# Optimization experiments

Hardware: AMD Instinct MI355X
Metric: run time of the kernel (lower is better)

## Reference

```python
import jax, jax.numpy as jnp
import numpy as np

B, T, D, H = 4, 1024, 1024, 16
HD = D // H  # 64
EPS = 1e-5


def _layernorm(x, g, b):
    mu = jnp.mean(x, axis=-1, keepdims=True)
    var = jnp.mean(jnp.square(x - mu), axis=-1, keepdims=True)
    return (x - mu) * jax.lax.rsqrt(var + EPS) * g + b


def _apply_rope(x, cos, sin):
    # x: (B, H, T, HD); cos/sin: (T, HD//2)
    d = x.shape[-1] // 2
    x1, x2 = x[..., :d], x[..., d:]
    cos = cos[None, None]
    sin = sin[None, None]
    return jnp.concatenate([x1 * cos - x2 * sin, x1 * sin + x2 * cos], axis=-1)


def setup_inputs() -> dict:
    key = jax.random.key(0)
    ks = jax.random.split(key, 8)
    s = 0.02
    x = jax.random.normal(ks[0], (B, T, D), jnp.float32)
    # RoPE tables
    pos = jnp.arange(T, dtype=jnp.float32)
    inv_freq = 1.0 / (10000.0 ** (jnp.arange(HD // 2, dtype=jnp.float32) / (HD // 2)))
    ang = pos[:, None] * inv_freq[None, :]  # (T, HD//2)
    rope_cos, rope_sin = jnp.cos(ang), jnp.sin(ang)
    # causal mask: True = masked out (module does ~attn_mask before SDPA)
    attn_mask = jnp.triu(jnp.ones((T, T), dtype=bool), k=1)
    params = dict(
        ln1_g=jnp.ones((D,), jnp.float32), ln1_b=jnp.zeros((D,), jnp.float32),
        w_qkv=jax.random.normal(ks[1], (D, 3 * D), jnp.float32) * s,
        b_qkv=jnp.zeros((3 * D,), jnp.float32),
        w_out=jax.random.normal(ks[2], (D, D), jnp.float32) * s,
        b_out=jnp.zeros((D,), jnp.float32),
        ln2_g=jnp.ones((D,), jnp.float32), ln2_b=jnp.zeros((D,), jnp.float32),
        w1=jax.random.normal(ks[3], (D, 4 * D), jnp.float32) * s,
        b1=jnp.zeros((4 * D,), jnp.float32),
        w2=jax.random.normal(ks[4], (4 * D, D), jnp.float32) * s,
        b2=jnp.zeros((D,), jnp.float32),
    )
    return dict(x=x, attn_mask=attn_mask, rope_cos=rope_cos, rope_sin=rope_sin, **params)


def reference(x, attn_mask, rope_cos, rope_sin, ln1_g, ln1_b, w_qkv, b_qkv,
              w_out, b_out, ln2_g, ln2_b, w1, b1, w2, b2):
    b, t, d = x.shape
    h = _layernorm(x, ln1_g, ln1_b)
    qkv = (h @ w_qkv + b_qkv).reshape(b, t, 3, H, HD)
    q, k, v = jnp.transpose(qkv, (2, 0, 3, 1, 4))  # each (B, H, T, HD)
    q = _apply_rope(q, rope_cos, rope_sin)
    k = _apply_rope(k, rope_cos, rope_sin)
    scale = 1.0 / jnp.sqrt(jnp.asarray(HD, x.dtype))
    scores = jnp.einsum('bhqd,bhkd->bhqk', q, k) * scale
    allowed = ~attn_mask  # True = attend
    neg = jnp.finfo(scores.dtype).min
    scores = jnp.where(allowed[None, None], scores, neg)
    probs = jax.nn.softmax(scores, axis=-1)
    attn = jnp.einsum('bhqk,bhkd->bhqd', probs, v)
    attn = jnp.transpose(attn, (0, 2, 1, 3)).reshape(b, t, d)
    x = x + (attn @ w_out + b_out)
    h2 = _layernorm(x, ln2_g, ln2_b)
    mlp = jax.nn.gelu(h2 @ w1 + b1, approximate=False) @ w2 + b2
    return x + mlp
```

## Files before the change

### kernel.cpp

```cpp
#include <hip/hip_runtime.h>
#include <hip/hip_bf16.h>
#include <cstdint>


typedef __bf16 bf16x8_t __attribute__((ext_vector_type(8)));
typedef float  f32x4_t  __attribute__((ext_vector_type(4)));

#define MFMA16(a, b, c) __builtin_amdgcn_mfma_f32_16x16x32_bf16((a), (b), (c), 0, 0, 0)

static constexpr int Bb = 4, T = 1024, D = 1024, NH = 16, HD = 64;
static constexpr int ROWS = Bb * T;
static constexpr int QKVN = 3 * D;

__device__ __forceinline__ float bf2f(__hip_bfloat16 v) { return __bfloat162float(v); }
__device__ __forceinline__ ushort f2bfbits(float v) {
    __hip_bfloat16 h = __float2bfloat16(v);
    return *reinterpret_cast<ushort*>(&h);
}
__device__ __forceinline__ float loadf(const void* p, size_t i, int isb16) {
    return isb16 ? bf2f(((const __hip_bfloat16*)p)[i]) : ((const float*)p)[i];
}
__device__ __forceinline__ int dtype16(const void* gref) {
    return (((const unsigned*)gref)[0] & 0xFFFFu) != 0u;
}
__device__ __forceinline__ void gld_lds16(const __hip_bfloat16* g, __hip_bfloat16* l) {
    __builtin_amdgcn_global_load_lds(
        (const __attribute__((address_space(1))) void*)g,
        (__attribute__((address_space(3))) void*)l, 16, 0, 0);
}

__device__ __forceinline__ void trans_tile(const void* B, __hip_bfloat16* BT,
                                           int K, int N, int k0, int n0, int isb16) {
    __shared__ ushort t[64][65];
#pragma unroll
    for (int it = 0; it < 16; ++it) {
        int idx = threadIdx.x + it * 256;
        int r = idx >> 6, c = idx & 63;
        t[c][r] = f2bfbits(loadf(B, (size_t)(k0 + r) * N + n0 + c, isb16));
    }
    __syncthreads();
#pragma unroll
    for (int it = 0; it < 16; ++it) {
        int idx = threadIdx.x + it * 256;
        int r = idx >> 6, c = idx & 63;
        reinterpret_cast<ushort*>(BT)[(size_t)(n0 + r) * K + k0 + c] = t[r][c];
    }
}

__global__ __launch_bounds__(256) void transpose_k(const void* __restrict__ B,
                                                   __hip_bfloat16* __restrict__ BT,
                                                   const void* __restrict__ gref,
                                                   int K, int N) {
    trans_tile(B, BT, K, N, blockIdx.y * 64, blockIdx.x * 64, dtype16(gref));
}

__global__ __launch_bounds__(256) void megatrans_k(const void* w_qkv, const void* w_out,
                                                   const void* w1, const void* w2,
                                                   __hip_bfloat16* wqkvT, __hip_bfloat16* woutT,
                                                   __hip_bfloat16* w1T, __hip_bfloat16* w2T,
                                                   const void* __restrict__ gref) {
    const int isb16 = dtype16(gref);
    int bid = blockIdx.x;
    const void* src; __hip_bfloat16* dst; int K, N, l;
    if (bid < 768)       { src = w_qkv; dst = wqkvT; K = 1024; N = 3072; l = bid; }
    else if (bid < 1024) { src = w_out; dst = woutT; K = 1024; N = 1024; l = bid - 768; }
    else if (bid < 2048) { src = w1;    dst = w1T;   K = 1024; N = 4096; l = bid - 1024; }
    else                 { src = w2;    dst = w2T;   K = 4096; N = 1024; l = bid - 2048; }
    const int nb = N / 64;
    trans_tile(src, dst, K, N, (l / nb) * 64, (l % nb) * 64, isb16);
}

__global__ __launch_bounds__(256) void ln_k(const void* __restrict__ x,
                                            const void* __restrict__ g,
                                            const void* __restrict__ bt,
                                            __hip_bfloat16* __restrict__ out,
                                            const void* __restrict__ gref) {
    const int isb16 = dtype16(gref);
    const int row = blockIdx.x, tid = threadIdx.x;
    const int lane = tid & 63, w = tid >> 6;

    float v[4];
    if (isb16) {
        ushort4 raw = reinterpret_cast<const ushort4*>((const __hip_bfloat16*)x + (size_t)row * D)[tid];
        v[0] = __uint_as_float(((unsigned)raw.x) << 16);
        v[1] = __uint_as_float(((unsigned)raw.y) << 16);
        v[2] = __uint_as_float(((unsigned)raw.z) << 16);
        v[3] = __uint_as_float(((unsigned)raw.w) << 16);
    } else {
        float4 f = reinterpret_cast<const float4*>((const float*)x + (size_t)row * D)[tid];
        v[0] = f.x; v[1] = f.y; v[2] = f.z; v[3] = f.w;
    }

    float s1 = v[0] + v[1] + v[2] + v[3];
    float s2 = v[0] * v[0] + v[1] * v[1] + v[2] * v[2] + v[3] * v[3];
#pragma unroll
    for (int off = 32; off >= 1; off >>= 1) {
        s1 += __shfl_xor(s1, off, 64);
        s2 += __shfl_xor(s2, off, 64);
    }
    __shared__ float r1[4], r2[4];
    if (lane == 0) { r1[w] = s1; r2[w] = s2; }
    __syncthreads();
    float t1 = r1[0] + r1[1] + r1[2] + r1[3];
    float t2 = r2[0] + r2[1] + r2[2] + r2[3];
    float mu  = t1 * (1.0f / D);
    float var = t2 * (1.0f / D) - mu * mu;
    float rstd = rsqrtf(var + 1e-5f);

    const int c = tid * 4;
#pragma unroll
    for (int j = 0; j < 4; j++) {
        float gv = loadf(g, c + j, isb16), bv = loadf(bt, c + j, isb16);
        out[(size_t)row * D + c + j] = __float2bfloat16((v[j] - mu) * rstd * gv + bv);
    }
}

template <int MODE, bool SPLIT>
__global__ __launch_bounds__(512, 2) void gemm256_k(const __hip_bfloat16* __restrict__ A,
                                                    const __hip_bfloat16* __restrict__ BT,
                                                    const void* __restrict__ bias,
                                                    void* __restrict__ C,
                                                    const void* __restrict__ gref,
                                                    int M, int N, int Kstride, int klen) {
    extern __shared__ __hip_bfloat16 LDSb[];

    const int tid  = threadIdx.x;
    const int lane = tid & 63, w = tid >> 6;
    const int quad = lane >> 4, l15 = lane & 15;
    const int n0 = blockIdx.x * 256, m0 = blockIdx.y * 256;
    const int wmL = (w >> 2) * 128;
    const int wnL = (w & 3) * 64;
    const int kbase = SPLIT ? blockIdx.z * klen : 0;
    const int NT = klen >> 5;

    const int L0 = w * 1024 + lane * 16;
    const int L1 = L0 + 8192;
    const int r0 = L0 >> 6,  k0e = ((L0 & 63) ^ (((L0 >> 9) & 1) << 5)) >> 1;
    const int r1 = L1 >> 6,  k1e = ((L1 & 63) ^ (((L1 >> 9) & 1) << 5)) >> 1;
    const __hip_bfloat16* AgS0 = A  + (size_t)(m0 + r0) * Kstride + kbase + k0e;
    const __hip_bfloat16* AgS1 = A  + (size_t)(m0 + r1) * Kstride + kbase + k1e;
    const __hip_bfloat16* BgS0 = BT + (size_t)(n0 + r0) * Kstride + kbase + k0e;
    const __hip_bfloat16* BgS1 = BT + (size_t)(n0 + r1) * Kstride + kbase + k1e;
    const int ldst0 = w * 512, ldst1 = w * 512 + 4096;

    const int kofs = (quad * 8) ^ ((l15 & 8) << 1);

    f32x4_t acc[8][4] = {};

#pragma unroll
    for (int t = 0; t < 3; ++t) {
        __hip_bfloat16* sA = LDSb + t * 8192;
        __hip_bfloat16* sB = LDSb + 32768 + t * 8192;
        const int ko = t * 32;
        gld_lds16(AgS0 + ko, sA + ldst0);
        gld_lds16(AgS1 + ko, sA + ldst1);
        gld_lds16(BgS0 + ko, sB + ldst0);
        gld_lds16(BgS1 + ko, sB + ldst1);
    }
    asm volatile("s_waitcnt vmcnt(8)" ::: "memory");
    __builtin_amdgcn_s_barrier();
    __builtin_amdgcn_sched_barrier(0);

    for (int t = 0; t < NT; ++t) {
        if (t) {
            if (t + 2 < NT)      { asm volatile("s_waitcnt vmcnt(8)" ::: "memory"); }
            else if (t + 1 < NT) { asm volatile("s_waitcnt vmcnt(4)" ::: "memory"); }
            else                 { asm volatile("s_waitcnt vmcnt(0)" ::: "memory"); }
            __builtin_amdgcn_s_barrier();
            __builtin_amdgcn_sched_barrier(0);
        }

        const __hip_bfloat16* sA = LDSb + (t & 3) * 8192;
        const __hip_bfloat16* sB = LDSb + 32768 + (t & 3) * 8192;
        const bool pf = (t + 3 < NT);
        const int sl = (t + 3) & 3;
        __hip_bfloat16* nA = LDSb + sl * 8192;
        __hip_bfloat16* nB = LDSb + 32768 + sl * 8192;
        const int ko = (t + 3) * 32;

        bf16x8_t a[4], b[4];
#pragma unroll
        for (int mf = 0; mf < 4; ++mf)
            a[mf] = *reinterpret_cast<const bf16x8_t*>(&sA[(wmL + mf * 16 + l15) * 32 + kofs]);
#pragma unroll
        for (int nf = 0; nf < 4; ++nf)
            b[nf] = *reinterpret_cast<const bf16x8_t*>(&sB[(wnL + nf * 16 + l15) * 32 + kofs]);
        if (pf) {
            gld_lds16(AgS0 + ko, nA + ldst0);
            gld_lds16(AgS1 + ko, nA + ldst1);
        }
        __builtin_amdgcn_sched_barrier(0);
        __builtin_amdgcn_s_barrier();
        asm volatile("s_waitcnt lgkmcnt(0)" ::: "memory");
        __builtin_amdgcn_sched_barrier(0);
        __builtin_amdgcn_s_setprio(1);
#pragma unroll
        for (int mf = 0; mf < 4; ++mf)
#pragma unroll
            for (int nf = 0; nf < 4; ++nf)
                acc[mf][nf] = MFMA16(a[mf], b[nf], acc[mf][nf]);
        __builtin_amdgcn_s_setprio(0);
        __builtin_amdgcn_sched_barrier(0);
        __builtin_amdgcn_s_barrier();

        bf16x8_t a2[4];
#pragma unroll
        for (int mf = 0; mf < 4; ++mf)
            a2[mf] = *reinterpret_cast<const bf16x8_t*>(&sA[(wmL + 64 + mf * 16 + l15) * 32 + kofs]);
        if (pf) {
            gld_lds16(BgS0 + ko, nB + ldst0);
            gld_lds16(BgS1 + ko, nB + ldst1);
        }
        __builtin_amdgcn_sched_barrier(0);
        asm volatile("s_waitcnt lgkmcnt(0)" ::: "memory");
        __builtin_amdgcn_sched_barrier(0);
        __builtin_amdgcn_s_setprio(1);
#pragma unroll
        for (int mf = 0; mf < 4; ++mf)
#pragma unroll
            for (int nf = 0; nf < 4; ++nf)
                acc[4 + mf][nf] = MFMA16(a2[mf], b[nf], acc[4 + mf][nf]);
        __builtin_amdgcn_s_setprio(0);
        __builtin_amdgcn_sched_barrier(0);
    }

    __syncthreads();

    __hip_bfloat16* Cb;
    if constexpr (SPLIT) {
        const int z = blockIdx.z;
        if (z == 0)      Cb = (__hip_bfloat16*)C;
        else if (z == 1) Cb = (__hip_bfloat16*)C + (size_t)M * N;
        else if (z == 2) Cb = (__hip_bfloat16*)const_cast<void*>(bias);
        else             Cb = (__hip_bfloat16*)const_cast<void*>(gref);
    } else {
        Cb = (__hip_bfloat16*)C;
    }
    const int isb16 = (MODE == 3) ? 0 : dtype16(gref);
    __hip_bfloat16* E = LDSb;
#pragma unroll
    for (int nf = 0; nf < 4; ++nf) {
        const int cc = wnL + nf * 16 + l15;
        const float bsv = (MODE == 3) ? 0.0f : loadf(bias, n0 + cc, isb16);
#pragma unroll
        for (int mf = 0; mf < 8; ++mf) {
            const int rbase = wmL + mf * 16 + quad * 4;
#pragma unroll
            for (int r = 0; r < 4; ++r) {
                const int rr = rbase + r;
                float v = acc[mf][nf][r] + bsv;
                if constexpr (MODE == 2)
                    v = 0.5f * v * (1.0f + erff(v * 0.70710678118654752f));
                E[rr * 256 + ((cc + (((rr >> 2) & 15) << 4)) & 255)] = __float2bfloat16(v);
            }
        }
    }
    __syncthreads();
#pragma unroll
    for (int it = 0; it < 16; ++it) {
        const int r = it * 16 + (tid >> 5), c = (tid & 31) * 8;
        const int cs = (c + (((r >> 2) & 15) << 4)) & 255;
        uint4 d = *reinterpret_cast<const uint4*>(&E[r * 256 + cs]);
        *reinterpret_cast<uint4*>(&Cb[(size_t)(m0 + r) * N + n0 + c]) = d;
    }
}

template <int MODE, bool SPLIT>
__global__ __launch_bounds__(256) void gemm_k(const __hip_bfloat16* __restrict__ A,
                                              const __hip_bfloat16* __restrict__ BT,
                                              const void* __restrict__ bias,
                                              void* __restrict__ C,
                                              const void* __restrict__ gref,
                                              int M, int N, int Kstride, int klen) {
    __shared__ __hip_bfloat16 LB[16384];

    const int tid  = threadIdx.x;
    const int lane = tid & 63, w = tid >> 6;
    const int quad = lane >> 4, l15 = lane & 15;
    const int n0 = blockIdx.x * 128, m0 = blockIdx.y * 128;
    const int wm = (w >> 1) * 64, wn = (w & 1) * 64;
    const int kbase = SPLIT ? blockIdx.z * klen : 0;

    const int srow = lane >> 2, skk = (lane & 3) * 8;
    const __hip_bfloat16* Ag = A  + (size_t)(m0 + w * 16 + srow) * Kstride + kbase + skk;
    const __hip_bfloat16* Bg = BT + (size_t)(n0 + w * 16 + srow) * Kstride + kbase + skk;
    const int lwb = (w * 16) * 32;

    f32x4_t acc[4][4] = {};

    gld_lds16(Ag,                LB + lwb);
    gld_lds16(Ag + 64 * Kstride, LB + lwb + 64 * 32);
    gld_lds16(Bg,                LB + 8192 + lwb);
    gld_lds16(Bg + 64 * Kstride, LB + 8192 + lwb + 64 * 32);
    __syncthreads();

    int p = 0;
    for (int k0 = 0; k0 < klen; k0 += 32) {
        if (k0 + 32 < klen) {
            __hip_bfloat16* An = LB + (p ^ 1) * 4096;
            __hip_bfloat16* Bn = LB + 8192 + (p ^ 1) * 4096;
            gld_lds16(Ag + k0 + 32,                An + lwb);
            gld_lds16(Ag + k0 + 32 + 64 * Kstride, An + lwb + 64 * 32);
            gld_lds16(Bg + k0 + 32,                Bn + lwb);
            gld_lds16(Bg + k0 + 32 + 64 * Kstride, Bn + lwb + 64 * 32);
        }

        const __hip_bfloat16* Ac = LB + p * 4096;
        const __hip_bfloat16* Bc = LB + 8192 + p * 4096;
        bf16x8_t af[4], bfr[4];
#pragma unroll
        for (int t = 0; t < 4; t++) {
            af[t]  = *reinterpret_cast<const bf16x8_t*>(&Ac[(wm + t * 16 + l15) * 32 + quad * 8]);
            bfr[t] = *reinterpret_cast<const bf16x8_t*>(&Bc[(wn + t * 16 + l15) * 32 + quad * 8]);
        }
#pragma unroll
        for (int i = 0; i < 4; i++)
#pragma unroll
            for (int j = 0; j < 4; j++)
                acc[i][j] = MFMA16(af[i], bfr[j], acc[i][j]);

        __syncthreads();
        p ^= 1;
    }

    __hip_bfloat16* Cb;
    if constexpr (SPLIT) {
        const int z = blockIdx.z;
        if (z == 0)      Cb = (__hip_bfloat16*)C;
        else if (z == 1) Cb = (__hip_bfloat16*)C + (size_t)M * N;
        else if (z == 2) Cb = (__hip_bfloat16*)const_cast<void*>(bias);
        else             Cb = (__hip_bfloat16*)const_cast<void*>(gref);
    } else {
        Cb = (__hip_bfloat16*)C;
    }
    const int isb16 = (MODE == 3) ? 0 : dtype16(gref);
    __hip_bfloat16* E = LB;
#pragma unroll
    for (int j = 0; j < 4; j++) {
        const int cc = wn + j * 16 + l15;
        const float bsv = (MODE == 3) ? 0.0f : loadf(bias, n0 + cc, isb16);
#pragma unroll
        for (int i = 0; i < 4; i++) {
            const int rbase = wm + i * 16 + quad * 4;
#pragma unroll
            for (int r = 0; r < 4; r++) {
                const int rr = rbase + r;
                float v = acc[i][j][r] + bsv;
                if constexpr (MODE == 2)
                    v = 0.5f * v * (1.0f + erff(v * 0.70710678118654752f));
                E[rr * 128 + ((cc + (((rr >> 2) & 7) << 4)) & 127)] = __float2bfloat16(v);
            }
        }
    }
    __syncthreads();
#pragma unroll
    for (int it = 0; it < 8; it++) {
        const int r = it * 16 + (tid >> 4), c = (tid & 15) * 8;
        const int cs = (c + (((r >> 2) & 7) << 4)) & 127;
        uint4 d = *reinterpret_cast<const uint4*>(&E[r * 128 + cs]);
        *reinterpret_cast<uint4*>(&Cb[(size_t)(m0 + r) * N + n0 + c]) = d;
    }
}

__global__ __launch_bounds__(256) void reduce4_k(const __hip_bfloat16* __restrict__ p0,
                                                 const __hip_bfloat16* __restrict__ p1,
                                                 const __hip_bfloat16* __restrict__ p2,
                                                 const __hip_bfloat16* __restrict__ p3,
                                                 const void* __restrict__ bias,
                                                 const void* __restrict__ res,
                                                 void* __restrict__ out,
                                                 const void* __restrict__ gref) {
    const int isb16 = dtype16(gref);
    const size_t i = ((size_t)blockIdx.x * 256 + threadIdx.x) * 4;
    ushort4 a = *reinterpret_cast<const ushort4*>(p0 + i);
    ushort4 b = *reinterpret_cast<const ushort4*>(p1 + i);
    ushort4 c = *reinterpret_cast<const ushort4*>(p2 + i);
    ushort4 d = *reinterpret_cast<const ushort4*>(p3 + i);
    const int col = (int)(i & (D - 1));
    float v[4];
    v[0] = __uint_as_float((unsigned)a.x << 16) + __uint_as_float((unsigned)b.x << 16)
         + __uint_as_float((unsigned)c.x << 16) + __uint_as_float((unsigned)d.x << 16);
    v[1] = __uint_as_float((unsigned)a.y << 16) + __uint_as_float((unsigned)b.y << 16)
         + __uint_as_float((unsigned)c.y << 16) + __uint_as_float((unsigned)d.y << 16);
    v[2] = __uint_as_float((unsigned)a.z << 16) + __uint_as_float((unsigned)b.z << 16)
         + __uint_as_float((unsigned)c.z << 16) + __uint_as_float((unsigned)d.z << 16);
    v[3] = __uint_as_float((unsigned)a.w << 16) + __uint_as_float((unsigned)b.w << 16)
         + __uint_as_float((unsigned)c.w << 16) + __uint_as_float((unsigned)d.w << 16);
#pragma unroll
    for (int j = 0; j < 4; j++)
        v[j] += loadf(bias, col + j, isb16) + loadf(res, i + j, isb16);
    if (isb16) {
        ushort4 o;
        o.x = f2bfbits(v[0]); o.y = f2bfbits(v[1]); o.z = f2bfbits(v[2]); o.w = f2bfbits(v[3]);
        *reinterpret_cast<ushort4*>((__hip_bfloat16*)out + i) = o;
    } else {
        float4 o = {v[0], v[1], v[2], v[3]};
        *reinterpret_cast<float4*>((float*)out + i) = o;
    }
}

__global__ __launch_bounds__(256) void gemm64_k(const __hip_bfloat16* __restrict__ A,
                                                const __hip_bfloat16* __restrict__ BT,
                                                const void* __restrict__ bias,
                                                const void* __restrict__ res,
                                                void* __restrict__ C,
                                                const void* __restrict__ gref,
                                                int M, int N, int K, int crow0) {
    __shared__ __hip_bfloat16 LB64[12288];

    const int tid  = threadIdx.x;
    const int lane = tid & 63, w = tid >> 6;
    const int quad = lane >> 4, l15 = lane & 15;
    const int n0 = blockIdx.x * 64, m0 = blockIdx.y * 128;
    const int wm = (w >> 1) * 64, wn = (w & 1) * 32;

    const int srow = lane >> 2, skk = (lane & 3) * 8;
    const __hip_bfloat16* Ag = A  + (size_t)(m0 + w * 16 + srow) * K + skk;
    const __hip_bfloat16* Bg = BT + (size_t)(n0 + w * 16 + srow) * K + skk;
    const int lwb = (w * 16) * 32;

    f32x4_t acc[4][2] = {};

    gld_lds16(Ag,          LB64 + lwb);
    gld_lds16(Ag + 64 * K, LB64 + lwb + 64 * 32);
    gld_lds16(Bg,          LB64 + 8192 + lwb);
    __syncthreads();

    int p = 0;
    for (int k0 = 0; k0 < K; k0 += 32) {
        if (k0 + 32 < K) {
            __hip_bfloat16* An = LB64 + (p ^ 1) * 4096;
            __hip_bfloat16* Bn = LB64 + 8192 + (p ^ 1) * 2048;
            gld_lds16(Ag + k0 + 32,          An + lwb);
            gld_lds16(Ag + k0 + 32 + 64 * K, An + lwb + 64 * 32);
            gld_lds16(Bg + k0 + 32,          Bn + lwb);
        }

        const __hip_bfloat16* Ac = LB64 + p * 4096;
        const __hip_bfloat16* Bc = LB64 + 8192 + p * 2048;
        bf16x8_t af[4], bfr[2];
#pragma unroll
        for (int t = 0; t < 4; t++)
            af[t]  = *reinterpret_cast<const bf16x8_t*>(&Ac[(wm + t * 16 + l15) * 32 + quad * 8]);
#pragma unroll
        for (int t = 0; t < 2; t++)
            bfr[t] = *reinterpret_cast<const bf16x8_t*>(&Bc[(wn + t * 16 + l15) * 32 + quad * 8]);
#pragma unroll
        for (int i = 0; i < 4; i++)
#pragma unroll
            for (int j = 0; j < 2; j++)
                acc[i][j] = MFMA16(af[i], bfr[j], acc[i][j]);

        __syncthreads();
        p ^= 1;
    }

    const int isb16 = dtype16(gref);
#pragma unroll
    for (int j = 0; j < 2; j++) {
        const int col = n0 + wn + j * 16 + l15;
        const float bsv = loadf(bias, col, isb16);
#pragma unroll
        for (int i = 0; i < 4; i++) {
            const int rbase = m0 + wm + i * 16 + quad * 4;
#pragma unroll
            for (int r = 0; r < 4; r++) {
                const size_t gr = (size_t)(crow0 + rbase + r);
                float v = acc[i][j][r] + bsv + loadf(res, gr * N + col, isb16);
                if (isb16) ((__hip_bfloat16*)C)[gr * N + col] = __float2bfloat16(v);
                else       ((float*)C)[gr * N + col] = v;
            }
        }
    }
}

__global__ __launch_bounds__(256) void ropevt_k(__hip_bfloat16* __restrict__ qkv,
                                                const void* __restrict__ rc,
                                                const void* __restrict__ rs,
                                                __hip_bfloat16* __restrict__ vT,
                                                const void* __restrict__ gref) {
    const int bid = blockIdx.x;
    if (bid < 8192) {
        const int isb16 = dtype16(gref);
        const int id = bid * 256 + threadIdx.x;
        const int d  = id & 31;
        const int h  = (id >> 5) & 15;
        const int t  = (id >> 9) & 1023;
        const int b  = id >> 19;
        const float c = loadf(rc, t * 32 + d, isb16);
        const float s = loadf(rs, t * 32 + d, isb16);
        __hip_bfloat16* base = qkv + ((size_t)(b * T + t)) * QKVN + h * HD + d;
        float x1 = bf2f(base[0]), x2 = bf2f(base[32]);
        base[0]  = __float2bfloat16((x1 * c - x2 * s) * 0.125f);
        base[32] = __float2bfloat16((x1 * s + x2 * c) * 0.125f);
        float y1 = bf2f(base[D]), y2 = bf2f(base[D + 32]);
        base[D]      = __float2bfloat16(y1 * c - y2 * s);
        base[D + 32] = __float2bfloat16(y1 * s + y2 * c);
    } else {
        __shared__ ushort t[64][65];
        const int l = bid - 8192;
        const int t0 = (l & 15) * 64, bh = l >> 4;
        const int b = bh >> 4, h = bh & 15;
        const __hip_bfloat16* src = qkv + ((size_t)b * T) * QKVN + 2 * D + h * HD;
#pragma unroll
        for (int it = 0; it < 16; ++it) {
            int idx = threadIdx.x + it * 256;
            int r = idx >> 6, d = idx & 63;
            t[d][r] = *reinterpret_cast<const ushort*>(src + (size_t)(t0 + r) * QKVN + d);
        }
        __syncthreads();
#pragma unroll
        for (int it = 0; it < 16; ++it) {
            int idx = threadIdx.x + it * 256;
            int r = idx >> 6, c = idx & 63;
            reinterpret_cast<ushort*>(vT)[((size_t)bh * 64 + r) * T + t0 + c] = t[r][c];
        }
    }
}

__global__ __launch_bounds__(256) void flash_k(const __hip_bfloat16* __restrict__ qkv,
                                               const __hip_bfloat16* __restrict__ vT,
                                               __hip_bfloat16* __restrict__ out) {
    __shared__ __hip_bfloat16 Qs[2][64 * 32];
    __shared__ __hip_bfloat16 Ks[2][2][64 * 32];
    __shared__ __hip_bfloat16 Vs[2][2][64 * 32];
    __shared__ __hip_bfloat16 Ps[4][2][16 * 32];

    const int tid = threadIdx.x;
    const int bid = blockIdx.x;
    const int qt = 15 - (bid >> 6);
    const int bh = bid & 63;
    const int b = bh >> 4, h = bh & 15;
    const int q0 = qt * 64;
    const int lane = tid & 63, w = tid >> 6, quad = lane >> 4, l15 = lane & 15;
    const int srow = lane >> 2, skk = (lane & 3) * 8;

    const __hip_bfloat16* qg = qkv + ((size_t)(b * T) + q0 + w * 16 + srow) * QKVN + h * HD + skk;
    const __hip_bfloat16* kg = qkv + ((size_t)(b * T) + w * 16 + srow) * QKVN + D + h * HD + skk;
    const __hip_bfloat16* vg = vT + ((size_t)bh * 64 + w * 16 + srow) * T + skk;

    gld_lds16(qg,      &Qs[0][(w * 16) * 32]);
    gld_lds16(qg + 32, &Qs[1][(w * 16) * 32]);
    gld_lds16(kg,      &Ks[0][0][(w * 16) * 32]);
    gld_lds16(kg + 32, &Ks[0][1][(w * 16) * 32]);
    gld_lds16(vg,      &Vs[0][0][(w * 16) * 32]);
    gld_lds16(vg + 32, &Vs[0][1][(w * 16) * 32]);
    __syncthreads();

    const bf16x8_t aq0 = *reinterpret_cast<const bf16x8_t*>(&Qs[0][(w * 16 + l15) * 32 + quad * 8]);
    const bf16x8_t aq1 = *reinterpret_cast<const bf16x8_t*>(&Qs[1][(w * 16 + l15) * 32 + quad * 8]);

    float m_run[4], l_run[4];
    f32x4_t o[4] = {};
#pragma unroll
    for (int i = 0; i < 4; i++) { m_run[i] = -1e30f; l_run[i] = 0.0f; }

    int p = 0;
    for (int kt = 0; kt <= qt; kt++) {
        if (kt < qt) {
            const size_t ko = (size_t)(kt + 1) * 64;
            gld_lds16(kg + ko * QKVN,      &Ks[p ^ 1][0][(w * 16) * 32]);
            gld_lds16(kg + ko * QKVN + 32, &Ks[p ^ 1][1][(w * 16) * 32]);
            gld_lds16(vg + ko,             &Vs[p ^ 1][0][(w * 16) * 32]);
            gld_lds16(vg + ko + 32,        &Vs[p ^ 1][1][(w * 16) * 32]);
        }

        f32x4_t s[4];
#pragma unroll
        for (int c = 0; c < 4; c++) {
            f32x4_t z = {};
            bf16x8_t k0f = *reinterpret_cast<const bf16x8_t*>(&Ks[p][0][(c * 16 + l15) * 32 + quad * 8]);
            bf16x8_t k1f = *reinterpret_cast<const bf16x8_t*>(&Ks[p][1][(c * 16 + l15) * 32 + quad * 8]);
            z = MFMA16(aq0, k0f, z);
            z = MFMA16(aq1, k1f, z);
            s[c] = z;
        }

        if (kt == qt) {
#pragma unroll
            for (int c = 0; c < 4; c++)
#pragma unroll
                for (int i = 0; i < 4; i++) {
                    int rr = w * 16 + quad * 4 + i;
                    int cc = c * 16 + l15;
                    if (cc > rr) s[c][i] = -1e30f;
                }
        }

        float mnew[4], alpha[4];
#pragma unroll
        for (int i = 0; i < 4; i++) {
            float mx = fmaxf(fmaxf(s[0][i], s[1][i]), fmaxf(s[2][i], s[3][i]));
#pragma unroll
            for (int off = 1; off < 16; off <<= 1) mx = fmaxf(mx, __shfl_xor(mx, off, 64));
            mnew[i] = fmaxf(m_run[i], mx);
            alpha[i] = __expf(m_run[i] - mnew[i]);
            m_run[i] = mnew[i];
        }
#pragma unroll
        for (int c = 0; c < 4; c++)
#pragma unroll
            for (int i = 0; i < 4; i++) s[c][i] = __expf(s[c][i] - mnew[i]);
#pragma unroll
        for (int i = 0; i < 4; i++) {
            float sm = s[0][i] + s[1][i] + s[2][i] + s[3][i];
#pragma unroll
            for (int off = 1; off < 16; off <<= 1) sm += __shfl_xor(sm, off, 64);
            l_run[i] = l_run[i] * alpha[i] + sm;
#pragma unroll
            for (int od = 0; od < 4; od++) o[od][i] *= alpha[i];
        }

#pragma unroll
        for (int c = 0; c < 4; c++)
#pragma unroll
            for (int i = 0; i < 4; i++)
                Ps[w][c >> 1][(quad * 4 + i) * 32 + (c & 1) * 16 + l15] =
                    __float2bfloat16(s[c][i]);

        bf16x8_t ap0 = *reinterpret_cast<const bf16x8_t*>(&Ps[w][0][l15 * 32 + quad * 8]);
        bf16x8_t ap1 = *reinterpret_cast<const bf16x8_t*>(&Ps[w][1][l15 * 32 + quad * 8]);
#pragma unroll
        for (int od = 0; od < 4; od++) {
            bf16x8_t v0f = *reinterpret_cast<const bf16x8_t*>(&Vs[p][0][(od * 16 + l15) * 32 + quad * 8]);
            bf16x8_t v1f = *reinterpret_cast<const bf16x8_t*>(&Vs[p][1][(od * 16 + l15) * 32 + quad * 8]);
            o[od] = MFMA16(ap0, v0f, o[od]);
            o[od] = MFMA16(ap1, v1f, o[od]);
        }

        __syncthreads();
        p ^= 1;
    }

#pragma unroll
    for (int od = 0; od < 4; od++)
#pragma unroll
        for (int i = 0; i < 4; i++) {
            int row = q0 + w * 16 + quad * 4 + i;
            int col = h * HD + od * 16 + l15;
            float v = o[od][i] / l_run[i];
            out[((size_t)b * T + row) * D + col] = __float2bfloat16(v);
        }
}

extern "C" void kernel_launch(void* const* d_in, const int* in_sizes, int n_in,
                              void* d_out, int out_size, void* d_ws, size_t ws_size,
                              hipStream_t stream) {
    const int o = (in_sizes[1] == T * (HD / 2)) ? 1 : 2;
    const void* x     = d_in[0];
    const void* rc    = d_in[o + 0];
    const void* rs    = d_in[o + 1];
    const void* ln1g  = d_in[o + 2];
    const void* ln1b  = d_in[o + 3];
    const void* w_qkv = d_in[o + 4];
    const void* b_qkv = d_in[o + 5];
    const void* w_out = d_in[o + 6];
    const void* b_out = d_in[o + 7];
    const void* ln2g  = d_in[o + 8];
    const void* ln2b  = d_in[o + 9];
    const void* w1    = d_in[o + 10];
    const void* b1    = d_in[o + 11];
    const void* w2    = d_in[o + 12];
    const void* b2    = d_in[o + 13];

    char* ws = (char*)d_ws;
    const size_t MB = 1024 * 1024;

    static bool attr_done = false;
    if (!attr_done) {
        hipFuncSetAttribute(reinterpret_cast<const void*>(&gemm256_k<0, false>),
                            hipFuncAttributeMaxDynamicSharedMemorySize, 131072);
        hipFuncSetAttribute(reinterpret_cast<const void*>(&gemm256_k<2, false>),
                            hipFuncAttributeMaxDynamicSharedMemorySize, 131072);
        hipFuncSetAttribute(reinterpret_cast<const void*>(&gemm256_k<3, true>),
                            hipFuncAttributeMaxDynamicSharedMemorySize, 131072);
        attr_done = true;
    }

    if (ws_size >= 72 * MB + 256) {
        __hip_bfloat16* bufA  = (__hip_bfloat16*)(ws + 256);
        __hip_bfloat16* qkvb  = (__hip_bfloat16*)(ws + 8 * MB + 256);
        __hip_bfloat16* vTb   = (__hip_bfloat16*)(ws + 32 * MB + 256);
        __hip_bfloat16* mid   = qkvb;
        __hip_bfloat16* wqkvT = (__hip_bfloat16*)(ws + 40 * MB + 256);
        __hip_bfloat16* woutT = (__hip_bfloat16*)(ws + 46 * MB + 256);
        __hip_bfloat16* w1T   = (__hip_bfloat16*)(ws + 48 * MB + 256);
        __hip_bfloat16* w2T   = (__hip_bfloat16*)(ws + 56 * MB + 256);
        __hip_bfloat16* part0 = (__hip_bfloat16*)(ws + 40 * MB + 256);
        __hip_bfloat16* part2 = (__hip_bfloat16*)(ws + 64 * MB + 256);
        __hip_bfloat16* part1 = (__hip_bfloat16*)(ws + 48 * MB + 256);
        __hip_bfloat16* part3 = bufA;

        megatrans_k<<<3072, 256, 0, stream>>>(w_qkv, w_out, w1, w2,
                                              wqkvT, woutT, w1T, w2T, ln1g);
        ln_k<<<ROWS, 256, 0, stream>>>(x, ln1g, ln1b, bufA, ln1g);
        gemm256_k<0, false><<<dim3(QKVN / 256, ROWS / 256), 512, 131072, stream>>>(
            bufA, wqkvT, b_qkv, qkvb, ln1g, ROWS, QKVN, D, D);
        ropevt_k<<<8192 + 1024, 256, 0, stream>>>(qkvb, rc, rs, vTb, ln1g);
        flash_k<<<16 * Bb * NH, 256, 0, stream>>>(qkvb, vTb, bufA);
        gemm64_k<<<dim3(D / 64, ROWS / 128), 256, 0, stream>>>(bufA, woutT, b_out, x,
                                                               d_out, ln1g, ROWS, D, D, 0);
        ln_k<<<ROWS, 256, 0, stream>>>(d_out, ln2g, ln2b, bufA, ln1g);
        gemm256_k<2, false><<<dim3(4 * D / 256, ROWS / 256), 512, 131072, stream>>>(
            bufA, w1T, b1, mid, ln1g, ROWS, 4 * D, D, D);
        gemm256_k<3, true><<<dim3(D / 256, ROWS / 256, 4), 512, 131072, stream>>>(
            mid, w2T, part2, part0, part3, ROWS, D, 4 * D, D);
        reduce4_k<<<(ROWS * D) / (256 * 4), 256, 0, stream>>>(part0, part1, part2, part3,
                                                              b2, d_out, d_out, ln1g);
    } else {
        __hip_bfloat16* bufA  = (__hip_bfloat16*)(ws + 256);
        __hip_bfloat16* qkvb  = (__hip_bfloat16*)(ws + 8 * MB + 256);
        __hip_bfloat16* wqkvT = (__hip_bfloat16*)(ws + 32 * MB + 256);
        __hip_bfloat16* vTb   = (__hip_bfloat16*)(ws + 32 * MB + 256);
        __hip_bfloat16* woutT = (__hip_bfloat16*)(ws + 8 * MB + 256);
        __hip_bfloat16* w1T   = (__hip_bfloat16*)(ws + 8 * MB + 256);
        __hip_bfloat16* w2T   = (__hip_bfloat16*)(ws + 16 * MB + 256);
        __hip_bfloat16* mid   = (__hip_bfloat16*)(ws + 24 * MB + 256);

        transpose_k<<<dim3(QKVN / 64, D / 64), 256, 0, stream>>>(w_qkv, wqkvT, ln1g, D, QKVN);
        ln_k<<<ROWS, 256, 0, stream>>>(x, ln1g, ln1b, bufA, ln1g);
        gemm_k<0, false><<<dim3(QKVN / 128, ROWS / 128), 256, 0, stream>>>(
            bufA, wqkvT, b_qkv, qkvb, ln1g, ROWS, QKVN, D, D);
        ropevt_k<<<8192 + 1024, 256, 0, stream>>>(qkvb, rc, rs, vTb, ln1g);
        flash_k<<<16 * Bb * NH, 256, 0, stream>>>(qkvb, vTb, bufA);
        transpose_k<<<dim3(D / 64, D / 64), 256, 0, stream>>>(w_out, woutT, ln1g, D, D);
        gemm64_k<<<dim3(D / 64, ROWS / 128), 256, 0, stream>>>(bufA, woutT, b_out, x,
                                                               d_out, ln1g, ROWS, D, D, 0);
        ln_k<<<ROWS, 256, 0, stream>>>(d_out, ln2g, ln2b, bufA, ln1g);
        transpose_k<<<dim3(4 * D / 64, D / 64), 256, 0, stream>>>(w1, w1T, ln1g, D, 4 * D);
        transpose_k<<<dim3(D / 64, 4 * D / 64), 256, 0, stream>>>(w2, w2T, ln1g, 4 * D, D);
        for (int c = 0; c < 2; c++) {
            const int ro = c * 2048;
            gemm_k<2, false><<<dim3(4 * D / 128, 2048 / 128), 256, 0, stream>>>(
                bufA + (size_t)ro * D, w1T, b1, mid, ln1g, 2048, 4 * D, D, D);
            gemm64_k<<<dim3(D / 64, 2048 / 128), 256, 0, stream>>>(mid, w2T, b2, d_out,
                                                                   d_out, ln1g, 2048, D, 4 * D, ro);
        }
    }
}
```

Baseline: 374.5 us.

## Restructure GEMM main loop to K=64 double-buffered four-phase pipeline with XCD-aware tile remap

```diff
diff --git a/kernel.cpp b/kernel.cpp
--- a/kernel.cpp
+++ b/kernel.cpp
@@ -127,68 +127,71 @@
     const int tid  = threadIdx.x;
     const int lane = tid & 63, w = tid >> 6;
     const int quad = lane >> 4, l15 = lane & 15;
-    const int n0 = blockIdx.x * 256, m0 = blockIdx.y * 256;
+
+    const int gx = gridDim.x;
+    const int nwg = gx * gridDim.y;
+    const int id = (int)blockIdx.y * gx + (int)blockIdx.x;
+    const int cpx = nwg >> 3;
+    const int sid = (id & 7) * cpx + (id >> 3);
+    const int n0 = (sid % gx) * 256, m0 = (sid / gx) * 256;
+
     const int wmL = (w >> 2) * 128;
     const int wnL = (w & 3) * 64;
     const int kbase = SPLIT ? blockIdx.z * klen : 0;
-    const int NT = klen >> 5;
-
-    const int L0 = w * 1024 + lane * 16;
-    const int L1 = L0 + 8192;
-    const int r0 = L0 >> 6,  k0e = ((L0 & 63) ^ (((L0 >> 9) & 1) << 5)) >> 1;
-    const int r1 = L1 >> 6,  k1e = ((L1 & 63) ^ (((L1 >> 9) & 1) << 5)) >> 1;
-    const __hip_bfloat16* AgS0 = A  + (size_t)(m0 + r0) * Kstride + kbase + k0e;
-    const __hip_bfloat16* AgS1 = A  + (size_t)(m0 + r1) * Kstride + kbase + k1e;
-    const __hip_bfloat16* BgS0 = BT + (size_t)(n0 + r0) * Kstride + kbase + k0e;
-    const __hip_bfloat16* BgS1 = BT + (size_t)(n0 + r1) * Kstride + kbase + k1e;
-    const int ldst0 = w * 512, ldst1 = w * 512 + 4096;
-
-    const int kofs = (quad * 8) ^ ((l15 & 8) << 1);
+    const int NT = klen >> 6;
+
+    const int gcol = 8 * ((lane & 7) ^ ((lane >> 3) & 7));
+    const __hip_bfloat16* AgS = A  + (size_t)(m0 + w * 8 + (lane >> 3)) * Kstride + kbase + gcol;
+    const __hip_bfloat16* BgS = BT + (size_t)(n0 + w * 8 + (lane >> 3)) * Kstride + kbase + gcol;
+    const int ldst = w * 512;
+
+    auto stgA = [&](int tt, int hi) {
+        __hip_bfloat16* d = LDSb + (tt & 1) * 16384 + hi * 8192 + ldst;
+        const __hip_bfloat16* g = AgS + (size_t)(hi * 128) * Kstride + (size_t)tt * 64;
+        gld_lds16(g,                          d);
+        gld_lds16(g + (size_t)64 * Kstride,   d + 4096);
+    };
+    auto stgB = [&](int tt, int hi) {
+        __hip_bfloat16* d = LDSb + 32768 + (tt & 1) * 16384 + hi * 8192 + ldst;
+        const __hip_bfloat16* g = BgS + (size_t)(hi * 128) * Kstride + (size_t)tt * 64;
+        gld_lds16(g,                          d);
+        gld_lds16(g + (size_t)64 * Kstride,   d + 4096);
+    };
+
+    const int cSw = (quad * 8) ^ ((l15 & 7) << 3);
+    auto rdA = [&](int as_, int row, int kk) -> bf16x8_t {
+        return *reinterpret_cast<const bf16x8_t*>(&LDSb[as_ + row * 64 + (cSw ^ (kk << 5))]);
+    };
+    auto rdB = [&](int bs_, int row, int kk) -> bf16x8_t {
+        return *reinterpret_cast<const bf16x8_t*>(&LDSb[bs_ + row * 64 + (cSw ^ (kk << 5))]);
+    };
 
     f32x4_t acc[8][4] = {};
 
-#pragma unroll
-    for (int t = 0; t < 3; ++t) {
-        __hip_bfloat16* sA = LDSb + t * 8192;
-        __hip_bfloat16* sB = LDSb + 32768 + t * 8192;
-        const int ko = t * 32;
-        gld_lds16(AgS0 + ko, sA + ldst0);
-        gld_lds16(AgS1 + ko, sA + ldst1);
-        gld_lds16(BgS0 + ko, sB + ldst0);
-        gld_lds16(BgS1 + ko, sB + ldst1);
-    }
-    asm volatile("s_waitcnt vmcnt(8)" ::: "memory");
+    stgA(0, 0); stgA(0, 1); stgB(0, 0); stgB(0, 1);
+    if (NT > 1) { stgB(1, 0); stgB(1, 1); }
+    if (NT > 1) { asm volatile("s_waitcnt vmcnt(4)" ::: "memory"); }
+    else        { asm volatile("s_waitcnt vmcnt(0)" ::: "memory"); }
     __builtin_amdgcn_s_barrier();
     __builtin_amdgcn_sched_barrier(0);
 
     for (int t = 0; t < NT; ++t) {
-        if (t) {
-            if (t + 2 < NT)      { asm volatile("s_waitcnt vmcnt(8)" ::: "memory"); }
-            else if (t + 1 < NT) { asm volatile("s_waitcnt vmcnt(4)" ::: "memory"); }
-            else                 { asm volatile("s_waitcnt vmcnt(0)" ::: "memory"); }
-            __builtin_amdgcn_s_barrier();
-            __builtin_amdgcn_sched_barrier(0);
-        }
-
-        const __hip_bfloat16* sA = LDSb + (t & 3) * 8192;
-        const __hip_bfloat16* sB = LDSb + 32768 + (t & 3) * 8192;
-        const bool pf = (t + 3 < NT);
-        const int sl = (t + 3) & 3;
-        __hip_bfloat16* nA = LDSb + sl * 8192;
-        __hip_bfloat16* nB = LDSb + 32768 + sl * 8192;
-        const int ko = (t + 3) * 32;
-
-        bf16x8_t a[4], b[4];
+        const int as = (t & 1) * 16384;
+        const int bs = 32768 + (t & 1) * 16384;
+        bf16x8_t aF[8], bF[8];
+
 #pragma unroll
         for (int mf = 0; mf < 4; ++mf)
-            a[mf] = *reinterpret_cast<const bf16x8_t*>(&sA[(wmL + mf * 16 + l15) * 32 + kofs]);
-#pragma unroll
-        for (int nf = 0; nf < 4; ++nf)
-            b[nf] = *reinterpret_cast<const bf16x8_t*>(&sB[(wnL + nf * 16 + l15) * 32 + kofs]);
-        if (pf) {
-            gld_lds16(AgS0 + ko, nA + ldst0);
-            gld_lds16(AgS1 + ko, nA + ldst1);
-        }
+#pragma unroll
+            for (int kk = 0; kk < 2; ++kk)
+                aF[mf * 2 + kk] = rdA(as, wmL + mf * 16 + l15, kk);
+#pragma unroll
+        for (int nf = 0; nf < 2; ++nf)
+#pragma unroll
+            for (int kk = 0; kk < 2; ++kk)
+                bF[nf * 2 + kk] = rdB(bs, wnL + nf * 16 + l15, kk);
+        if (t + 1 < NT) stgA(t + 1, 0);
+        asm volatile("s_waitcnt lgkmcnt(8)" ::: "memory");
         __builtin_amdgcn_sched_barrier(0);
         __builtin_amdgcn_s_barrier();
         asm volatile("s_waitcnt lgkmcnt(0)" ::: "memory");
@@ -197,31 +200,74 @@
 #pragma unroll
         for (int mf = 0; mf < 4; ++mf)
 #pragma unroll
-            for (int nf = 0; nf < 4; ++nf)
-                acc[mf][nf] = MFMA16(a[mf], b[nf], acc[mf][nf]);
+            for (int nf = 0; nf < 2; ++nf)
+#pragma unroll
+                for (int kk = 0; kk < 2; ++kk)
+                    acc[mf][nf] = MFMA16(aF[mf * 2 + kk], bF[nf * 2 + kk], acc[mf][nf]);
         __builtin_amdgcn_s_setprio(0);
         __builtin_amdgcn_sched_barrier(0);
         __builtin_amdgcn_s_barrier();
 
-        bf16x8_t a2[4];
+#pragma unroll
+        for (int nf = 2; nf < 4; ++nf)
+#pragma unroll
+            for (int kk = 0; kk < 2; ++kk)
+                bF[nf * 2 + kk] = rdB(bs, wnL + nf * 16 + l15, kk);
+        if (t + 1 < NT) stgA(t + 1, 1);
+        __builtin_amdgcn_sched_barrier(0);
+        __builtin_amdgcn_s_barrier();
+        asm volatile("s_waitcnt lgkmcnt(0)" ::: "memory");
+        __builtin_amdgcn_sched_barrier(0);
+        __builtin_amdgcn_s_setprio(1);
 #pragma unroll
         for (int mf = 0; mf < 4; ++mf)
-            a2[mf] = *reinterpret_cast<const bf16x8_t*>(&sA[(wmL + 64 + mf * 16 + l15) * 32 + kofs]);
-        if (pf) {
-            gld_lds16(BgS0 + ko, nB + ldst0);
-            gld_lds16(BgS1 + ko, nB + ldst1);
-        }
-        __builtin_amdgcn_sched_barrier(0);
+#pragma unroll
+            for (int nf = 2; nf < 4; ++nf)
+#pragma unroll
+                for (int kk = 0; kk < 2; ++kk)
+                    acc[mf][nf] = MFMA16(aF[mf * 2 + kk], bF[nf * 2 + kk], acc[mf][nf]);
+        __builtin_amdgcn_s_setprio(0);
+        __builtin_amdgcn_sched_barrier(0);
+        __builtin_amdgcn_s_barrier();
+
+#pragma unroll
+        for (int mf = 0; mf < 4; ++mf)
+#pragma unroll
+            for (int kk = 0; kk < 2; ++kk)
+                aF[mf * 2 + kk] = rdA(as, wmL + 64 + mf * 16 + l15, kk);
+        if (t + 2 < NT) stgB(t + 2, 0);
+        __builtin_amdgcn_sched_barrier(0);
+        __builtin_amdgcn_s_barrier();
         asm volatile("s_waitcnt lgkmcnt(0)" ::: "memory");
         __builtin_amdgcn_sched_barrier(0);
         __builtin_amdgcn_s_setprio(1);
 #pragma unroll
         for (int mf = 0; mf < 4; ++mf)
 #pragma unroll
-            for (int nf = 0; nf < 4; ++nf)
-                acc[4 + mf][nf] = MFMA16(a2[mf], b[nf], acc[4 + mf][nf]);
+            for (int nf = 0; nf < 2; ++nf)
+#pragma unroll
+                for (int kk = 0; kk < 2; ++kk)
+                    acc[4 + mf][nf] = MFMA16(aF[mf * 2 + kk], bF[nf * 2 + kk], acc[4 + mf][nf]);
         __builtin_amdgcn_s_setprio(0);
         __builtin_amdgcn_sched_barrier(0);
+        __builtin_amdgcn_s_barrier();
+
+        if (t + 2 < NT) stgB(t + 2, 1);
+        if (t + 2 < NT) { asm volatile("s_waitcnt vmcnt(4)" ::: "memory"); }
+        else            { asm volatile("s_waitcnt vmcnt(0)" ::: "memory"); }
+        __builtin_amdgcn_sched_barrier(0);
+        __builtin_amdgcn_s_barrier();
+        __builtin_amdgcn_s_setprio(1);
+#pragma unroll
+        for (int mf = 0; mf < 4; ++mf)
+#pragma unroll
+            for (int nf = 2; nf < 4; ++nf)
+#pragma unroll
+                for (int kk = 0; kk < 2; ++kk)
+                    acc[4 + mf][nf] = MFMA16(aF[mf * 2 + kk], bF[nf * 2 + kk], acc[4 + mf][nf]);
+        __builtin_amdgcn_s_setprio(0);
+        __builtin_amdgcn_sched_barrier(0);
+        __builtin_amdgcn_s_barrier();
     }
 
     __syncthreads();
```

Result: no change. 375.2 us (+0.2%).
